# Kernel optimization log

Measured on AMD Instinct MI355X. Metric: run time of the kernel, lower is better.

## Reference

```python
import jax, jax.numpy as jnp
import numpy as np

V, E, U, T, B = 32000, 256, 512, 32, 64

def setup_inputs() -> dict:
    key = jax.random.key(0)
    ks = jax.random.split(key, 12)
    return {
        "input_seq": jax.random.randint(ks[0], (B, T), 1, V),
        "target": jax.random.randint(ks[1], (B, T), 1, V),
        "encoder_output": jax.random.normal(ks[2], (B, T, U), jnp.float32),
        "enc_h": jax.random.normal(ks[3], (B, U), jnp.float32),
        "enc_c": jax.random.normal(ks[4], (B, U), jnp.float32),
        "emb": jax.random.normal(ks[5], (V, E), jnp.float32) * 0.02,
        "Wk": jax.random.normal(ks[6], (E, 4 * U), jnp.float32) * 0.05,
        "Wr": jax.random.normal(ks[7], (U, 4 * U), jnp.float32) * 0.05,
        "b": jnp.zeros((4 * U,), jnp.float32),
        "Wgen": jax.random.normal(ks[8], (2 * U + E, U), jnp.float32) * 0.05,
        "bgen": jnp.zeros((U,), jnp.float32),
    }


def _lstm(x, h0, c0, Wk, Wr, b):
    # x: [B,T,E]; Keras gate order i,f,c,o; returns seq of h [B,T,U], hT, cT
    xg = jnp.einsum('bte,eg->btg', x, Wk) + b  # precompute input projections
    def cell(carry, xg_t):
        h, c = carry
        g = xg_t + h @ Wr
        i, f, cc, o = jnp.split(g, 4, axis=-1)
        c_new = jax.nn.sigmoid(f) * c + jax.nn.sigmoid(i) * jnp.tanh(cc)
        h_new = jax.nn.sigmoid(o) * jnp.tanh(c_new)
        return (h_new, c_new), h_new
    (hT, cT), hs = jax.lax.scan(cell, (h0, c0), jnp.swapaxes(xg, 0, 1))
    return jnp.swapaxes(hs, 0, 1), hT, cT


def reference(input_seq, target, encoder_output, enc_h, enc_c, emb, Wk, Wr, b, Wgen, bgen):
    dec_in0 = emb[target]  # [B,T,E]
    def outer(carry, _):
        dec_in, h, c = carry
        outs, hT, cT = _lstm(dec_in, h, c, Wk, Wr, b)  # [B,T,U]
        h_b = jnp.broadcast_to(h[:, None, :], (B, T, U))  # pre-update state, per original
        feat = jnp.concatenate([encoder_output, h_b, dec_in], axis=-1)
        p_gen = jax.nn.sigmoid(feat @ Wgen + bgen)  # [B,T,U]
        idx = jnp.argmax(outs, axis=-1)  # greedy 'token' ids (as in original)
        new_in = emb[idx]
        return (new_in, hT, cT), (outs, p_gen, h, c)
    _, (dec_outs, p_gens, hs, cs) = jax.lax.scan(
        outer, (dec_in0, enc_h, enc_c), None, length=T - 1)
    return dec_outs, p_gens, hs, cs
```

## Files before the change

### kernel.cpp

```cpp
#include <hip/hip_runtime.h>
#include <math.h>

#define Bz 64
#define Tz 32
#define Ez 256
#define Uz 512
#define NITER 31
#define G4 2048
#define NBG 8
#define NUB 32
#define BPB 8
#define UPB 16
#define JPB 64

typedef unsigned long long ull;

__device__ __forceinline__ float sigf(float x) { return 1.f / (1.f + expf(-x)); }

#define AT_LOADF(p)    __hip_atomic_load((p), __ATOMIC_RELAXED, __HIP_MEMORY_SCOPE_AGENT)
#define AT_STOREF(p,v) __hip_atomic_store((p), (v), __ATOMIC_RELAXED, __HIP_MEMORY_SCOPE_AGENT)

__device__ __forceinline__ void bg_barrier(unsigned* fl, int ug, unsigned step, int tid) {
  asm volatile("s_waitcnt vmcnt(0)" ::: "memory");
  __syncthreads();
  if (tid == 0)
    __hip_atomic_store(&fl[ug * 16], step, __ATOMIC_RELAXED, __HIP_MEMORY_SCOPE_AGENT);
  if (tid < NUB) {
    unsigned v;
    do {
      v = __hip_atomic_fetch_add(&fl[tid * 16], 0u, __ATOMIC_RELAXED, __HIP_MEMORY_SCOPE_AGENT);
    } while (v < step);
  }
  __syncthreads();
}

__global__ __launch_bounds__(256) void gemm_f32(
    const float* __restrict__ A, const int* __restrict__ Arows, int lda,
    const float* __restrict__ Bm, int ldb, const float* __restrict__ bias,
    float* __restrict__ C, int N, int K)
{
  __shared__ __align__(16) float As[16][68];
  __shared__ __align__(16) float Bs[16][68];
  const int tid = threadIdx.x;
  const int bm = blockIdx.y, bn = blockIdx.x;
  const int tx = tid & 15, ty = tid >> 4;
  float acc[4][4] = {{0.f}};
  const int sm = tid >> 2, sk = (tid & 3) * 4;
  const int arow = Arows ? Arows[bm * 64 + sm] : (bm * 64 + sm);
  const float* Ap = A + (size_t)arow * lda + sk;
  const int bk = tid >> 4, bn4 = (tid & 15) * 4;
  const float* Bp = Bm + (size_t)bk * ldb + bn * 64 + bn4;
  for (int kk = 0; kk < K; kk += 16) {
    float4 av = *(const float4*)(Ap + kk);
    float4 bv = *(const float4*)(Bp + (size_t)kk * ldb);
    As[sk + 0][sm] = av.x; As[sk + 1][sm] = av.y;
    As[sk + 2][sm] = av.z; As[sk + 3][sm] = av.w;
    *(float4*)&Bs[bk][bn4] = bv;
    __syncthreads();
#pragma unroll
    for (int kt = 0; kt < 16; ++kt) {
      float4 a = *(const float4*)&As[kt][ty * 4];
      float4 b = *(const float4*)&Bs[kt][tx * 4];
      acc[0][0] += a.x * b.x; acc[0][1] += a.x * b.y; acc[0][2] += a.x * b.z; acc[0][3] += a.x * b.w;
      acc[1][0] += a.y * b.x; acc[1][1] += a.y * b.y; acc[1][2] += a.y * b.z; acc[1][3] += a.y * b.w;
      acc[2][0] += a.z * b.x; acc[2][1] += a.z * b.y; acc[2][2] += a.z * b.z; acc[2][3] += a.z * b.w;
      acc[3][0] += a.w * b.x; acc[3][1] += a.w * b.y; acc[3][2] += a.w * b.z; acc[3][3] += a.w * b.w;
    }
    __syncthreads();
  }
  const int cm = bm * 64 + ty * 4, cn = bn * 64 + tx * 4;
  float bc0 = bias ? bias[cn + 0] : 0.f;
  float bc1 = bias ? bias[cn + 1] : 0.f;
  float bc2 = bias ? bias[cn + 2] : 0.f;
  float bc3 = bias ? bias[cn + 3] : 0.f;
#pragma unroll
  for (int i = 0; i < 4; ++i) {
    float4 o;
    o.x = acc[i][0] + bc0; o.y = acc[i][1] + bc1;
    o.z = acc[i][2] + bc2; o.w = acc[i][3] + bc3;
    *(float4*)&C[(size_t)(cm + i) * N + cn] = o;
  }
}

__global__ void init_kernel(const float* __restrict__ enc_h, float* __restrict__ hbT,
                            unsigned* __restrict__ flags) {
  int i = blockIdx.x * blockDim.x + threadIdx.x;
  if (i < NBG * NUB * 16) flags[i] = 0u;
  if (i < Bz * Uz) {
    int u = i & 511, bb = i >> 9;
    int bg = bb >> 3, b = bb & 7;
    hbT[bg * 8192 + u * 8 + b] = enc_h[(size_t)bb * Uz + u];
  }
}

__global__ __launch_bounds__(512, 1) void decoder_persist(
    const float* __restrict__ Wr,
    const float* __restrict__ Wgen,
    const float* __restrict__ bgen,
    const float* __restrict__ enc_h,
    const float* __restrict__ enc_c,
    const float* __restrict__ embW,
    const float* __restrict__ xg0,
    const float* __restrict__ enc_part,
    const float* __restrict__ dec0,
    const float* __restrict__ decW,
    float* __restrict__ hbT,
    int*   __restrict__ idxbuf,
    unsigned* __restrict__ flags,
    float* __restrict__ out)
{
  __shared__ __align__(16) float WlT[512 * JPB];
  __shared__ __align__(16) float hred[4096];
  __shared__ __align__(16) float g_l[512];
  __shared__ __align__(16) float hW_l[128];

  const int tid = threadIdx.x;
  const int bid = blockIdx.x;
  const int bg = bid >> 5, ug = bid & 31;
  const int b0 = bg * BPB, u0 = ug * UPB;
  const int lane = tid & 63, wv_ = tid >> 6;

  float* out_dec = out;
  float* out_pg  = out + (size_t)NITER * Bz * Tz * Uz;
  float* out_hs  = out + 2 * (size_t)NITER * Bz * Tz * Uz;
  float* out_cs  = out_hs + (size_t)NITER * Bz * Uz;

  unsigned* fl = flags + bg * NUB * 16;
  unsigned bt_ = 0;

  for (int q = 0; q < 64; ++q) {
    int e = q * 512 + tid;
    int k = e >> 6, j = e & 63;
    WlT[k * 64 + j] = Wr[(size_t)k * G4 + (j >> 4) * Uz + u0 + (j & 15)];
  }

  const int kgrp = tid >> 5, tile = tid & 31;
  const int g_bt = tile >> 4, g_jt = tile & 15;
  const int t_t = tid >> 4, o_e = tid & 15;
  const int o_bl = (t_t >> 4) * 4 + (o_e >> 2);
  const int o_j  = (t_t & 15) * 4 + (o_e & 3);
  const int o_gcol = (o_j >> 4) * Uz + u0 + (o_j & 15);
  const int o_rbase = (b0 + o_bl) * Tz;
  const int p_b = tid >> 4, p_ul = tid & 15;

  float c_reg = 0.f, h_reg = 0.f;
  if (tid < 128) {
    c_reg = enc_c[(size_t)(b0 + p_b) * Uz + u0 + p_ul];
    h_reg = enc_h[(size_t)(b0 + p_b) * Uz + u0 + p_ul];
  }
  __syncthreads();

#pragma unroll 1
  for (int s = 0; s < NITER; ++s) {
    const int* idxp = idxbuf + ((s + 1) & 1) * 2048;
    int*       idxq = idxbuf + (s & 1) * 2048;

    {
      const ull* src = (const ull*)&hbT[bg * 8192];
      ull* dst = (ull*)hred;
#pragma unroll
      for (int q = 0; q < 2; ++q) {
        int u2 = tid + q * 512;
        ull v0 = __hip_atomic_load(&src[u2 * 2], __ATOMIC_RELAXED, __HIP_MEMORY_SCOPE_AGENT);
        ull v1 = __hip_atomic_load(&src[u2 * 2 + 1], __ATOMIC_RELAXED, __HIP_MEMORY_SCOPE_AGENT);
        dst[u2 * 2] = v0; dst[u2 * 2 + 1] = v1;
      }
    }
    if (tid < 128) {
      out_hs[((size_t)s * Bz + b0 + p_b) * Uz + u0 + p_ul] = h_reg;
      out_cs[((size_t)s * Bz + b0 + p_b) * Uz + u0 + p_ul] = c_reg;
    }
    float gv;
    if (s == 0) gv = xg0[(size_t)o_rbase * G4 + o_gcol];
    else {
      int iv = __hip_atomic_load(&idxp[o_rbase], __ATOMIC_RELAXED, __HIP_MEMORY_SCOPE_AGENT);
      gv = embW[(size_t)iv * G4 + o_gcol];
    }
    __syncthreads();

    {
      const int o = tid & 127, kp = tid >> 7;
      const int b = o >> 4, ul = o & 15;
      float a = 0.f;
#pragma unroll 8
      for (int k = kp * 128; k < kp * 128 + 128; ++k)
        a += hred[k * 8 + b] * Wgen[(size_t)(512 + k) * Uz + u0 + ul];
      g_l[kp * 128 + o] = a;
    }
    __syncthreads();
    if (tid < 128)
      hW_l[tid] = (g_l[tid] + g_l[tid + 128]) + (g_l[tid + 256] + g_l[tid + 384]);
    __syncthreads();

#pragma unroll 1
    for (int i = 0; i < 8; ++i) {
      int o = i * 512 + tid;
      int ul = o & 15, t = (o >> 4) & 31, b = o >> 9;
      int r = (b0 + b) * Tz + t;
      float dv;
      if (s == 0) dv = dec0[(size_t)r * Uz + u0 + ul];
      else {
        int iv = __hip_atomic_load(&idxp[r], __ATOMIC_RELAXED, __HIP_MEMORY_SCOPE_AGENT);
        dv = decW[(size_t)iv * Uz + u0 + ul];
      }
      float v = enc_part[(size_t)r * Uz + u0 + ul] + hW_l[b * 16 + ul] + dv + bgen[u0 + ul];
      out_pg[((size_t)(s * Bz + b0 + b) * Tz + t) * Uz + u0 + ul] = sigf(v);
    }
    __syncthreads();

#pragma unroll 1
    for (int t = 0; t < Tz; ++t) {
      float acc[4][4] = {{0.f}};
#pragma unroll 4
      for (int kk = 0; kk < 32; ++kk) {
        int k = kk * 16 + kgrp;
        float4 hv = *(const float4*)&hred[k * 8 + g_bt * 4];
        float4 wv = *(const float4*)&WlT[k * 64 + g_jt * 4];
        acc[0][0] += hv.x * wv.x; acc[0][1] += hv.x * wv.y; acc[0][2] += hv.x * wv.z; acc[0][3] += hv.x * wv.w;
        acc[1][0] += hv.y * wv.x; acc[1][1] += hv.y * wv.y; acc[1][2] += hv.y * wv.z; acc[1][3] += hv.y * wv.w;
        acc[2][0] += hv.z * wv.x; acc[2][1] += hv.z * wv.y; acc[2][2] += hv.z * wv.z; acc[2][3] += hv.z * wv.w;
        acc[3][0] += hv.w * wv.x; acc[3][1] += hv.w * wv.y; acc[3][2] += hv.w * wv.z; acc[3][3] += hv.w * wv.w;
      }
#pragma unroll
      for (int bi = 0; bi < 4; ++bi)
#pragma unroll
        for (int ji = 0; ji < 4; ++ji)
          acc[bi][ji] += __shfl_xor(acc[bi][ji], 32);
      __syncthreads();
      if (lane < 32) {
#pragma unroll
        for (int bi = 0; bi < 4; ++bi) {
          float4 o4; o4.x = acc[bi][0]; o4.y = acc[bi][1]; o4.z = acc[bi][2]; o4.w = acc[bi][3];
          *(float4*)&hred[wv_ * 512 + tile * 16 + bi * 4] = o4;
        }
      }
      __syncthreads();
      {
        float gsum = gv;
#pragma unroll
        for (int w = 0; w < 8; ++w) gsum += hred[w * 512 + t_t * 16 + o_e];
        g_l[o_bl * 64 + o_j] = gsum;
      }
      __syncthreads();
      if (tid < 128) {
        float gi = g_l[p_b * 64 +  0 + p_ul];
        float gf = g_l[p_b * 64 + 16 + p_ul];
        float gc = g_l[p_b * 64 + 32 + p_ul];
        float go = g_l[p_b * 64 + 48 + p_ul];
        c_reg = sigf(gf) * c_reg + sigf(gi) * tanhf(gc);
        float hn = sigf(go) * tanhf(c_reg);
        h_reg = hn;
        AT_STOREF(&hbT[bg * 8192 + ((t & 1) ^ 1) * 4096 + (u0 + p_ul) * 8 + p_b], hn);
        AT_STOREF(&out_dec[((size_t)(s * Bz + b0 + p_b) * Tz + t) * Uz + u0 + p_ul], hn);
      }
      bt_ += 1; bg_barrier(fl, ug, bt_, tid);
      if (t < Tz - 1) {
        const ull* src = (const ull*)&hbT[bg * 8192 + ((t & 1) ^ 1) * 4096];
        ull* dst = (ull*)hred;
#pragma unroll
        for (int q = 0; q < 2; ++q) {
          int u2 = tid + q * 512;
          ull v0 = __hip_atomic_load(&src[u2 * 2], __ATOMIC_RELAXED, __HIP_MEMORY_SCOPE_AGENT);
          ull v1 = __hip_atomic_load(&src[u2 * 2 + 1], __ATOMIC_RELAXED, __HIP_MEMORY_SCOPE_AGENT);
          dst[u2 * 2] = v0; dst[u2 * 2 + 1] = v1;
        }
        int r = o_rbase + t + 1;
        if (s == 0) gv = xg0[(size_t)r * G4 + o_gcol];
        else {
          int iv = __hip_atomic_load(&idxp[r], __ATOMIC_RELAXED, __HIP_MEMORY_SCOPE_AGENT);
          gv = embW[(size_t)iv * G4 + o_gcol];
        }
        __syncthreads();
      }
    }

    {
      int i = tid >> 6;
      int R = ug * 8 + i;
      int b = R >> 5, t = R & 31;
      const float* row = &out_dec[((size_t)(s * Bz + b0 + b) * Tz + t) * Uz];
      float bv = -3.4e38f; int bi_ = 0;
#pragma unroll
      for (int q = 0; q < 8; ++q) {
        int u = lane + q * 64;
        float v = AT_LOADF(&row[u]);
        if (v > bv) { bv = v; bi_ = u; }
      }
#pragma unroll
      for (int off = 1; off < 64; off <<= 1) {
        float ov = __shfl_xor(bv, off);
        int   oi = __shfl_xor(bi_, off);
        if (ov > bv || (ov == bv && oi < bi_)) { bv = ov; bi_ = oi; }
      }
      if (lane == 0)
        __hip_atomic_store(&idxq[(b0 + b) * Tz + t], bi_, __ATOMIC_RELAXED, __HIP_MEMORY_SCOPE_AGENT);
    }
    bt_ += 1; bg_barrier(fl, ug, bt_, tid);
  }
}

extern "C" void kernel_launch(void* const* d_in, const int* in_sizes, int n_in,
                              void* d_out, int out_size, void* d_ws, size_t ws_size,
                              hipStream_t stream) {
  const int*   target = (const int*)d_in[1];
  const float* enc    = (const float*)d_in[2];
  const float* enc_h  = (const float*)d_in[3];
  const float* enc_cp = (const float*)d_in[4];
  const float* emb    = (const float*)d_in[5];
  const float* Wk     = (const float*)d_in[6];
  const float* Wr     = (const float*)d_in[7];
  const float* bb     = (const float*)d_in[8];
  const float* Wgen   = (const float*)d_in[9];
  const float* bgen   = (const float*)d_in[10];
  float* out = (float*)d_out;

  float* ws = (float*)d_ws;
  float* hbT      = ws;
  float* embW     = ws + 65536;
  float* xg0      = ws + 1114112;
  float* enc_part = ws + 5308416;
  float* dec0     = ws + 6356992;
  float* decW     = ws + 7405568;
  int*   idxbuf   = (int*)(ws + 7667712);
  unsigned* flags = (unsigned*)(ws + 7671808);

  init_kernel<<<64, 512, 0, stream>>>(enc_h, hbT, flags);
  gemm_f32<<<dim3(32, 8), 256, 0, stream>>>(emb, nullptr, 256, Wk, 2048, bb, embW, 2048, 256);
  gemm_f32<<<dim3(32, 32), 256, 0, stream>>>(emb, target, 256, Wk, 2048, bb, xg0, 2048, 256);
  gemm_f32<<<dim3(8, 32), 256, 0, stream>>>(enc, nullptr, 512, Wgen, 512, nullptr, enc_part, 512, 512);
  gemm_f32<<<dim3(8, 32), 256, 0, stream>>>(emb, target, 256, Wgen + 1024 * 512, 512, nullptr, dec0, 512, 256);
  gemm_f32<<<dim3(8, 8), 256, 0, stream>>>(emb, nullptr, 256, Wgen + 1024 * 512, 512, nullptr, decW, 512, 256);

  decoder_persist<<<256, 512, 0, stream>>>(Wr, Wgen, bgen, enc_h, enc_cp, embW, xg0,
      enc_part, dec0, decW, hbT, idxbuf, flags, out);
}
```

Before: 5.486 ms.

## Ping-pong two batch groups per block to overlap recurrent steps with barriers

Each persistent block now owns two 4-batch groups (A and B) and alternates their recurrent GEMM steps. While one group's hidden state is being published and its flag barrier is pending, the block computes the other group, which aims to hide cross-block synchronization latency. Wr slices are kept in registers and Wgen slices in shared memory. The full-block barrier is replaced by a wavefront-level poll on per-group flags, and argmax indices are cached in LDS. In exchange, the flag protocol becomes more intricate and carries a risk of ordering or race bugs, and register pressure rises.

```diff
diff --git a/kernel.cpp b/kernel.cpp
--- a/kernel.cpp
+++ b/kernel.cpp
@@ -3,35 +3,25 @@
 
 #define Bz 64
 #define Tz 32
-#define Ez 256
 #define Uz 512
 #define NITER 31
 #define G4 2048
-#define NBG 8
-#define NUB 32
-#define BPB 8
-#define UPB 16
-#define JPB 64
 
 typedef unsigned long long ull;
 
 __device__ __forceinline__ float sigf(float x) { return 1.f / (1.f + expf(-x)); }
 
-#define AT_LOADF(p)    __hip_atomic_load((p), __ATOMIC_RELAXED, __HIP_MEMORY_SCOPE_AGENT)
-#define AT_STOREF(p,v) __hip_atomic_store((p), (v), __ATOMIC_RELAXED, __HIP_MEMORY_SCOPE_AGENT)
-
-__device__ __forceinline__ void bg_barrier(unsigned* fl, int ug, unsigned step, int tid) {
-  asm volatile("s_waitcnt vmcnt(0)" ::: "memory");
-  __syncthreads();
-  if (tid == 0)
-    __hip_atomic_store(&fl[ug * 16], step, __ATOMIC_RELAXED, __HIP_MEMORY_SCOPE_AGENT);
-  if (tid < NUB) {
-    unsigned v;
-    do {
-      v = __hip_atomic_fetch_add(&fl[tid * 16], 0u, __ATOMIC_RELAXED, __HIP_MEMORY_SCOPE_AGENT);
-    } while (v < step);
-  }
-  __syncthreads();
+#define AT_LOADF(p)   __hip_atomic_load((p), __ATOMIC_RELAXED, __HIP_MEMORY_SCOPE_AGENT)
+#define AT_LOADI(p)   __hip_atomic_load((p), __ATOMIC_RELAXED, __HIP_MEMORY_SCOPE_AGENT)
+#define AT_LOAD64(p)  __hip_atomic_load((p), __ATOMIC_RELAXED, __HIP_MEMORY_SCOPE_AGENT)
+#define AT_STORE(p,v) __hip_atomic_store((p), (v), __ATOMIC_RELAXED, __HIP_MEMORY_SCOPE_AGENT)
+
+__device__ __forceinline__ void poll32(unsigned* fl, unsigned target) {
+  int sl = threadIdx.x & 63;
+  unsigned v;
+  do {
+    v = __hip_atomic_fetch_add(&fl[sl * 16], 0u, __ATOMIC_RELAXED, __HIP_MEMORY_SCOPE_AGENT);
+  } while (__any((int)(v < target)));
 }
 
 __global__ __launch_bounds__(256) void gemm_f32(
@@ -82,16 +72,43 @@
   }
 }
 
-__global__ void init_kernel(const float* __restrict__ enc_h, float* __restrict__ hbT,
-                            unsigned* __restrict__ flags) {
+__global__ void init_kernel(unsigned* __restrict__ flags) {
   int i = blockIdx.x * blockDim.x + threadIdx.x;
-  if (i < NBG * NUB * 16) flags[i] = 0u;
-  if (i < Bz * Uz) {
-    int u = i & 511, bb = i >> 9;
-    int bg = bb >> 3, b = bb & 7;
-    hbT[bg * 8192 + u * 8 + b] = enc_h[(size_t)bb * Uz + u];
-  }
-}
+  if (i < 8192) flags[i] = 0u;
+}
+
+#define DO_GEMM(HRED, GIDX, GV)                                                          \
+  {                                                                                      \
+    float4 a0 = {0,0,0,0}, a1 = {0,0,0,0}, a2 = {0,0,0,0}, a3 = {0,0,0,0};               \
+    _Pragma("unroll")                                                                    \
+    for (int kk = 0; kk < 16; ++kk) {                                                    \
+      float4 hv = *(const float4*)&HRED[(kk * 32 + ks) * 4];                             \
+      a0.x += hv.x * w4[kk].x; a0.y += hv.x * w4[kk].y;                                  \
+      a0.z += hv.x * w4[kk].z; a0.w += hv.x * w4[kk].w;                                  \
+      a1.x += hv.y * w4[kk].x; a1.y += hv.y * w4[kk].y;                                  \
+      a1.z += hv.y * w4[kk].z; a1.w += hv.y * w4[kk].w;                                  \
+      a2.x += hv.z * w4[kk].x; a2.y += hv.z * w4[kk].y;                                  \
+      a2.z += hv.z * w4[kk].z; a2.w += hv.z * w4[kk].w;                                  \
+      a3.x += hv.w * w4[kk].x; a3.y += hv.w * w4[kk].y;                                  \
+      a3.z += hv.w * w4[kk].z; a3.w += hv.w * w4[kk].w;                                  \
+    }                                                                                    \
+    _Pragma("unroll")                                                                    \
+    for (int off = 2; off < 64; off <<= 1) {                                             \
+      a0.x += __shfl_xor(a0.x, off); a0.y += __shfl_xor(a0.y, off);                      \
+      a0.z += __shfl_xor(a0.z, off); a0.w += __shfl_xor(a0.w, off);                      \
+      a1.x += __shfl_xor(a1.x, off); a1.y += __shfl_xor(a1.y, off);                      \
+      a1.z += __shfl_xor(a1.z, off); a1.w += __shfl_xor(a1.w, off);                      \
+      a2.x += __shfl_xor(a2.x, off); a2.y += __shfl_xor(a2.y, off);                      \
+      a2.z += __shfl_xor(a2.z, off); a2.w += __shfl_xor(a2.w, off);                      \
+      a3.x += __shfl_xor(a3.x, off); a3.y += __shfl_xor(a3.y, off);                      \
+      a3.z += __shfl_xor(a3.z, off); a3.w += __shfl_xor(a3.w, off);                      \
+    }                                                                                    \
+    if (lane < 32) {                                                                     \
+      float4 rw = (b_w == 0) ? a0 : (b_w == 1) ? a1 : (b_w == 2) ? a2 : a3;              \
+      float val = (ji_w == 0) ? rw.x : (ji_w == 1) ? rw.y : (ji_w == 2) ? rw.z : rw.w;   \
+      g_l[GIDX][b_w][jwr] = val + (GV);                                                  \
+    }                                                                                    \
+  }
 
 __global__ __launch_bounds__(512, 1) void decoder_persist(
     const float* __restrict__ Wr,
@@ -109,193 +126,200 @@
     unsigned* __restrict__ flags,
     float* __restrict__ out)
 {
-  __shared__ __align__(16) float WlT[512 * JPB];
-  __shared__ __align__(16) float hred[4096];
-  __shared__ __align__(16) float g_l[512];
-  __shared__ __align__(16) float hW_l[128];
+  __shared__ __align__(16) float hredA[2048];
+  __shared__ __align__(16) float hredB[2048];
+  __shared__ __align__(16) float Wgenl[8192];
+  __shared__ float g_l[2][4][68];
+  __shared__ float hW_l[128];
+  __shared__ float redl[512];
+  __shared__ int   idx_l[8][32];
+  __shared__ float bgen_l[16];
 
   const int tid = threadIdx.x;
   const int bid = blockIdx.x;
-  const int bg = bid >> 5, ug = bid & 31;
-  const int b0 = bg * BPB, u0 = ug * UPB;
-  const int lane = tid & 63, wv_ = tid >> 6;
+  const int pr = bid >> 5, ug = bid & 31;
+  const int bA0 = pr * 4, bB0 = 32 + pr * 4;
+  const int u0 = ug * 16;
+  const int w = tid >> 6, lane = tid & 63;
+  const int ks = lane >> 1, jsub = lane & 1;
+  const int b_w = ks >> 2, ji_w = ks & 3;
+  const int jloc = w * 8 + jsub * 4;
+  const int gcol0 = (jloc >> 4) * Uz + u0 + (jloc & 15);
+  const int jwr = jloc + ji_w;
+  const int gcolw = gcol0 + ji_w;
+  const int p_b = lane >> 4, p_ul = lane & 15;
 
   float* out_dec = out;
   float* out_pg  = out + (size_t)NITER * Bz * Tz * Uz;
   float* out_hs  = out + 2 * (size_t)NITER * Bz * Tz * Uz;
   float* out_cs  = out_hs + (size_t)NITER * Bz * Uz;
 
-  unsigned* fl = flags + bg * NUB * 16;
-  unsigned bt_ = 0;
-
-  for (int q = 0; q < 64; ++q) {
-    int e = q * 512 + tid;
-    int k = e >> 6, j = e & 63;
-    WlT[k * 64 + j] = Wr[(size_t)k * G4 + (j >> 4) * Uz + u0 + (j & 15)];
-  }
-
-  const int kgrp = tid >> 5, tile = tid & 31;
-  const int g_bt = tile >> 4, g_jt = tile & 15;
-  const int t_t = tid >> 4, o_e = tid & 15;
-  const int o_bl = (t_t >> 4) * 4 + (o_e >> 2);
-  const int o_j  = (t_t & 15) * 4 + (o_e & 3);
-  const int o_gcol = (o_j >> 4) * Uz + u0 + (o_j & 15);
-  const int o_rbase = (b0 + o_bl) * Tz;
-  const int p_b = tid >> 4, p_ul = tid & 15;
-
-  float c_reg = 0.f, h_reg = 0.f;
-  if (tid < 128) {
-    c_reg = enc_c[(size_t)(b0 + p_b) * Uz + u0 + p_ul];
-    h_reg = enc_h[(size_t)(b0 + p_b) * Uz + u0 + p_ul];
-  }
+  unsigned* flA = flags + (pr * 2 + 0) * 512;
+  unsigned* flB = flags + (pr * 2 + 1) * 512;
+  float* hbTp = hbT + pr * 8192;
+
+  float4 w4[16];
+#pragma unroll
+  for (int kk = 0; kk < 16; ++kk)
+    w4[kk] = *(const float4*)&Wr[(size_t)(kk * 32 + ks) * G4 + gcol0];
+  for (int q = 0; q < 16; ++q) {
+    int e = q * 512 + tid, k = e >> 4, ul = e & 15;
+    Wgenl[k * 16 + ul] = Wgen[(size_t)(512 + k) * Uz + u0 + ul];
+  }
+  if (tid < 16) bgen_l[tid] = bgen[u0 + tid];
+  {
+    int k = tid;
+#pragma unroll
+    for (int b = 0; b < 4; ++b) {
+      hredA[k * 4 + b] = enc_h[(size_t)(bA0 + b) * Uz + k];
+      hredB[k * 4 + b] = enc_h[(size_t)(bB0 + b) * Uz + k];
+    }
+  }
+  float c_reg = 0.f;
+  if (w == 0) c_reg = enc_c[(size_t)(bA0 + p_b) * Uz + u0 + p_ul];
+  if (w == 1) c_reg = enc_c[(size_t)(bB0 + p_b) * Uz + u0 + p_ul];
   __syncthreads();
 
 #pragma unroll 1
   for (int s = 0; s < NITER; ++s) {
     const int* idxp = idxbuf + ((s + 1) & 1) * 2048;
     int*       idxq = idxbuf + (s & 1) * 2048;
-
+    const unsigned base = 33u * s;
+
+    if (s > 0) {
+      if (w == 1 && lane < 32) poll32(flA, base);
+      __syncthreads();
+      if (tid < 256) {
+        int pb = tid >> 5, t = tid & 31;
+        int batch = (pb < 4) ? bA0 + pb : bB0 + (pb - 4);
+        idx_l[pb][t] = AT_LOADI(&idxp[batch * Tz + t]);
+      }
+    }
     {
-      const ull* src = (const ull*)&hbT[bg * 8192];
-      ull* dst = (ull*)hred;
-#pragma unroll
-      for (int q = 0; q < 2; ++q) {
-        int u2 = tid + q * 512;
-        ull v0 = __hip_atomic_load(&src[u2 * 2], __ATOMIC_RELAXED, __HIP_MEMORY_SCOPE_AGENT);
-        ull v1 = __hip_atomic_load(&src[u2 * 2 + 1], __ATOMIC_RELAXED, __HIP_MEMORY_SCOPE_AGENT);
-        dst[u2 * 2] = v0; dst[u2 * 2 + 1] = v1;
-      }
-    }
-    if (tid < 128) {
-      out_hs[((size_t)s * Bz + b0 + p_b) * Uz + u0 + p_ul] = h_reg;
-      out_cs[((size_t)s * Bz + b0 + p_b) * Uz + u0 + p_ul] = c_reg;
-    }
-    float gv;
-    if (s == 0) gv = xg0[(size_t)o_rbase * G4 + o_gcol];
-    else {
-      int iv = __hip_atomic_load(&idxp[o_rbase], __ATOMIC_RELAXED, __HIP_MEMORY_SCOPE_AGENT);
-      gv = embW[(size_t)iv * G4 + o_gcol];
-    }
-    __syncthreads();
-
-    {
-      const int o = tid & 127, kp = tid >> 7;
-      const int b = o >> 4, ul = o & 15;
+      int g = tid >> 8, r6 = tid & 255, kq = r6 >> 6, l6 = r6 & 63;
+      int b = l6 >> 4, ul = l6 & 15;
+      const float* hr = g ? hredB : hredA;
       float a = 0.f;
 #pragma unroll 8
-      for (int k = kp * 128; k < kp * 128 + 128; ++k)
-        a += hred[k * 8 + b] * Wgen[(size_t)(512 + k) * Uz + u0 + ul];
-      g_l[kp * 128 + o] = a;
+      for (int k = kq * 128; k < kq * 128 + 128; ++k)
+        a += hr[k * 4 + b] * Wgenl[k * 16 + ul];
+      redl[tid] = a;
     }
     __syncthreads();
-    if (tid < 128)
-      hW_l[tid] = (g_l[tid] + g_l[tid + 128]) + (g_l[tid + 256] + g_l[tid + 384]);
+    if (tid < 128) {
+      int g = tid >> 6, l6 = tid & 63;
+      hW_l[tid] = (redl[g * 256 + l6] + redl[g * 256 + 64 + l6]) +
+                  (redl[g * 256 + 128 + l6] + redl[g * 256 + 192 + l6]);
+    }
+    if (w < 2) {
+      int batch = (w == 0 ? bA0 : bB0) + p_b;
+      const float* hr = w ? hredB : hredA;
+      out_hs[((size_t)s * Bz + batch) * Uz + u0 + p_ul] = hr[(u0 + p_ul) * 4 + p_b];
+      out_cs[((size_t)s * Bz + batch) * Uz + u0 + p_ul] = c_reg;
+    }
     __syncthreads();
-
 #pragma unroll 1
     for (int i = 0; i < 8; ++i) {
       int o = i * 512 + tid;
-      int ul = o & 15, t = (o >> 4) & 31, b = o >> 9;
-      int r = (b0 + b) * Tz + t;
-      float dv;
-      if (s == 0) dv = dec0[(size_t)r * Uz + u0 + ul];
-      else {
-        int iv = __hip_atomic_load(&idxp[r], __ATOMIC_RELAXED, __HIP_MEMORY_SCOPE_AGENT);
-        dv = decW[(size_t)iv * Uz + u0 + ul];
-      }
-      float v = enc_part[(size_t)r * Uz + u0 + ul] + hW_l[b * 16 + ul] + dv + bgen[u0 + ul];
-      out_pg[((size_t)(s * Bz + b0 + b) * Tz + t) * Uz + u0 + ul] = sigf(v);
-    }
-    __syncthreads();
+      int ul = o & 15, t = (o >> 4) & 31, pb = o >> 9;
+      int batch = (pb < 4) ? bA0 + pb : bB0 + (pb - 4);
+      size_t r = (size_t)batch * Tz + t;
+      float dv = (s == 0) ? dec0[r * Uz + u0 + ul]
+                          : decW[(size_t)idx_l[pb][t] * Uz + u0 + ul];
+      float v = enc_part[r * Uz + u0 + ul] + hW_l[(pb >> 2) * 64 + (pb & 3) * 16 + ul]
+              + dv + bgen_l[ul];
+      out_pg[(((size_t)s * Bz + batch) * Tz + t) * Uz + u0 + ul] = sigf(v);
+    }
 
 #pragma unroll 1
     for (int t = 0; t < Tz; ++t) {
-      float acc[4][4] = {{0.f}};
-#pragma unroll 4
-      for (int kk = 0; kk < 32; ++kk) {
-        int k = kk * 16 + kgrp;
-        float4 hv = *(const float4*)&hred[k * 8 + g_bt * 4];
-        float4 wv = *(const float4*)&WlT[k * 64 + g_jt * 4];
-        acc[0][0] += hv.x * wv.x; acc[0][1] += hv.x * wv.y; acc[0][2] += hv.x * wv.z; acc[0][3] += hv.x * wv.w;
-        acc[1][0] += hv.y * wv.x; acc[1][1] += hv.y * wv.y; acc[1][2] += hv.y * wv.z; acc[1][3] += hv.y * wv.w;
-        acc[2][0] += hv.z * wv.x; acc[2][1] += hv.z * wv.y; acc[2][2] += hv.z * wv.z; acc[2][3] += hv.z * wv.w;
-        acc[3][0] += hv.w * wv.x; acc[3][1] += hv.w * wv.y; acc[3][2] += hv.w * wv.z; acc[3][3] += hv.w * wv.w;
-      }
-#pragma unroll
-      for (int bi = 0; bi < 4; ++bi)
-#pragma unroll
-        for (int ji = 0; ji < 4; ++ji)
-          acc[bi][ji] += __shfl_xor(acc[bi][ji], 32);
-      __syncthreads();
+      const int gt = s * Tz + t;
+      float gvA = 0.f;
       if (lane < 32) {
-#pragma unroll
-        for (int bi = 0; bi < 4; ++bi) {
-          float4 o4; o4.x = acc[bi][0]; o4.y = acc[bi][1]; o4.z = acc[bi][2]; o4.w = acc[bi][3];
-          *(float4*)&hred[wv_ * 512 + tile * 16 + bi * 4] = o4;
-        }
-      }
-      __syncthreads();
-      {
-        float gsum = gv;
-#pragma unroll
-        for (int w = 0; w < 8; ++w) gsum += hred[w * 512 + t_t * 16 + o_e];
-        g_l[o_bl * 64 + o_j] = gsum;
-      }
-      __syncthreads();
-      if (tid < 128) {
-        float gi = g_l[p_b * 64 +  0 + p_ul];
-        float gf = g_l[p_b * 64 + 16 + p_ul];
-        float gc = g_l[p_b * 64 + 32 + p_ul];
-        float go = g_l[p_b * 64 + 48 + p_ul];
+        int r = (bA0 + b_w) * Tz + t;
+        gvA = (s == 0) ? xg0[(size_t)r * G4 + gcolw]
+                       : embW[(size_t)idx_l[b_w][t] * G4 + gcolw];
+      }
+      if (w == 1 && lane < 32) poll32(flB, base + t);
+      DO_GEMM(hredA, 0, gvA);
+      __syncthreads();
+      float gvB = 0.f;
+      if (lane < 32) {
+        int r = (bB0 + b_w) * Tz + t;
+        gvB = (s == 0) ? xg0[(size_t)r * G4 + gcolw]
+                       : embW[(size_t)idx_l[4 + b_w][t] * G4 + gcolw];
+      }
+      if (w == 0) {
+        float gi = g_l[0][p_b][p_ul],      gf = g_l[0][p_b][16 + p_ul];
+        float gc = g_l[0][p_b][32 + p_ul], go = g_l[0][p_b][48 + p_ul];
         c_reg = sigf(gf) * c_reg + sigf(gi) * tanhf(gc);
         float hn = sigf(go) * tanhf(c_reg);
-        h_reg = hn;
-        AT_STOREF(&hbT[bg * 8192 + ((t & 1) ^ 1) * 4096 + (u0 + p_ul) * 8 + p_b], hn);
-        AT_STOREF(&out_dec[((size_t)(s * Bz + b0 + p_b) * Tz + t) * Uz + u0 + p_ul], hn);
-      }
-      bt_ += 1; bg_barrier(fl, ug, bt_, tid);
-      if (t < Tz - 1) {
-        const ull* src = (const ull*)&hbT[bg * 8192 + ((t & 1) ^ 1) * 4096];
-        ull* dst = (ull*)hred;
-#pragma unroll
-        for (int q = 0; q < 2; ++q) {
-          int u2 = tid + q * 512;
-          ull v0 = __hip_atomic_load(&src[u2 * 2], __ATOMIC_RELAXED, __HIP_MEMORY_SCOPE_AGENT);
-          ull v1 = __hip_atomic_load(&src[u2 * 2 + 1], __ATOMIC_RELAXED, __HIP_MEMORY_SCOPE_AGENT);
-          dst[u2 * 2] = v0; dst[u2 * 2 + 1] = v1;
+        int parw = (gt + 1) & 1;
+        AT_STORE(&hbTp[(parw * 2 + 0) * 2048 + (u0 + p_ul) * 4 + p_b], hn);
+        AT_STORE(&out_dec[(((size_t)s * Bz + bA0 + p_b) * Tz + t) * Uz + u0 + p_ul], hn);
+        asm volatile("s_waitcnt vmcnt(0)" ::: "memory");
+        if (lane == 0) AT_STORE(&flA[ug * 16], base + t + 1);
+      } else if (w >= 2 && w < 6 && gt > 0) {
+        int st = tid - 128;
+        const ull* src = (const ull*)&hbTp[((gt & 1) * 2 + 1) * 2048];
+        ull* dst = (ull*)hredB;
+#pragma unroll
+        for (int q = 0; q < 4; ++q) dst[st * 4 + q] = AT_LOAD64(&src[st * 4 + q]);
+      }
+      __syncthreads();
+      if (w == 6 && lane < 32) poll32(flA, base + t + 1);
+      DO_GEMM(hredB, 1, gvB);
+      __syncthreads();
+      if (w == 1) {
+        float gi = g_l[1][p_b][p_ul],      gf = g_l[1][p_b][16 + p_ul];
+        float gc = g_l[1][p_b][32 + p_ul], go = g_l[1][p_b][48 + p_ul];
+        c_reg = sigf(gf) * c_reg + sigf(gi) * tanhf(gc);
+        float hn = sigf(go) * tanhf(c_reg);
+        int parw = (gt + 1) & 1;
+        AT_STORE(&hbTp[(parw * 2 + 1) * 2048 + (u0 + p_ul) * 4 + p_b], hn);
+        AT_STORE(&out_dec[(((size_t)s * Bz + bB0 + p_b) * Tz + t) * Uz + u0 + p_ul], hn);
+        asm volatile("s_waitcnt vmcnt(0)" ::: "memory");
+        if (lane == 0) AT_STORE(&flB[ug * 16], base + t + 1);
+      } else if (w >= 2 && w < 6) {
+        int st = tid - 128;
+        const ull* src = (const ull*)&hbTp[(((gt + 1) & 1) * 2 + 0) * 2048];
+        ull* dst = (ull*)hredA;
+#pragma unroll
+        for (int q = 0; q < 4; ++q) dst[st * 4 + q] = AT_LOAD64(&src[st * 4 + q]);
+      }
+      __syncthreads();
+    }
+
+    if (s < NITER - 1) {
+      if (w == 1 && lane < 32) poll32(flB, base + 32);
+      __syncthreads();
+      {
+        int R = ug * 8 + w;
+        int pb = R >> 5, t = R & 31;
+        int batch = (pb < 4) ? bA0 + pb : bB0 + (pb - 4);
+        const float* row = &out_dec[(((size_t)s * Bz + batch) * Tz + t) * Uz];
+        float bv = -3.4e38f; int bi = 0;
+#pragma unroll
+        for (int q = 0; q < 8; ++q) {
+          int u = lane + q * 64;
+          float v = AT_LOADF(&row[u]);
+          if (v > bv) { bv = v; bi = u; }
         }
-        int r = o_rbase + t + 1;
-        if (s == 0) gv = xg0[(size_t)r * G4 + o_gcol];
-        else {
-          int iv = __hip_atomic_load(&idxp[r], __ATOMIC_RELAXED, __HIP_MEMORY_SCOPE_AGENT);
-          gv = embW[(size_t)iv * G4 + o_gcol];
+#pragma unroll
+        for (int off = 1; off < 64; off <<= 1) {
+          float ov = __shfl_xor(bv, off);
+          int   oi = __shfl_xor(bi, off);
+          if (ov > bv || (ov == bv && oi < bi)) { bv = ov; bi = oi; }
         }
-        __syncthreads();
-      }
-    }
-
-    {
-      int i = tid >> 6;
-      int R = ug * 8 + i;
-      int b = R >> 5, t = R & 31;
-      const float* row = &out_dec[((size_t)(s * Bz + b0 + b) * Tz + t) * Uz];
-      float bv = -3.4e38f; int bi_ = 0;
-#pragma unroll
-      for (int q = 0; q < 8; ++q) {
-        int u = lane + q * 64;
-        float v = AT_LOADF(&row[u]);
-        if (v > bv) { bv = v; bi_ = u; }
-      }
-#pragma unroll
-      for (int off = 1; off < 64; off <<= 1) {
-        float ov = __shfl_xor(bv, off);
-        int   oi = __shfl_xor(bi_, off);
-        if (ov > bv || (ov == bv && oi < bi_)) { bv = ov; bi_ = oi; }
-      }
-      if (lane == 0)
-        __hip_atomic_store(&idxq[(b0 + b) * Tz + t], bi_, __ATOMIC_RELAXED, __HIP_MEMORY_SCOPE_AGENT);
-    }
-    bt_ += 1; bg_barrier(fl, ug, bt_, tid);
+        if (lane == 0) AT_STORE(&idxq[batch * Tz + t], bi);
+      }
+      asm volatile("s_waitcnt vmcnt(0)" ::: "memory");
+      __syncthreads();
+      if (tid == 0) {
+        AT_STORE(&flA[ug * 16], base + 33);
+        AT_STORE(&flB[ug * 16], base + 33);
+      }
+    }
   }
 }
 
@@ -324,7 +348,7 @@
   int*   idxbuf   = (int*)(ws + 7667712);
   unsigned* flags = (unsigned*)(ws + 7671808);
 
-  init_kernel<<<64, 512, 0, stream>>>(enc_h, hbT, flags);
+  init_kernel<<<16, 512, 0, stream>>>(flags);
   gemm_f32<<<dim3(32, 8), 256, 0, stream>>>(emb, nullptr, 256, Wk, 2048, bb, embW, 2048, 256);
   gemm_f32<<<dim3(32, 32), 256, 0, stream>>>(emb, target, 256, Wk, 2048, bb, xg0, 2048, 256);
   gemm_f32<<<dim3(8, 32), 256, 0, stream>>>(enc, nullptr, 512, Wgen, 512, nullptr, enc_part, 512, 512);
```

After: 7.849 ms. 1.43x slower.
